# Kernel tuning notes

Measured on AMD Instinct MI355X. Metric: run time of the kernel, lower is better.

Reference implementation:

```python
import jax, jax.numpy as jnp
import numpy as np

N = 50000      # nodes
E = 800000     # edges per view (before self loops)
F_IN = 256     # node feature dim
H = 4          # attention heads
C = 128        # hidden dim (per-head out_channels; concat=False -> mean over heads)
V = 3          # views
NEG_SLOPE = 0.2


def gat_view(x, edge_index, W, a_src, a_dst, b):
    """PyG-style GATConv(heads=H, concat=False) + ELU. Adds self loops."""
    n = x.shape[0]
    loops = jnp.arange(n, dtype=edge_index.dtype)
    src = jnp.concatenate([edge_index[0], loops])  # [E+N]
    dst = jnp.concatenate([edge_index[1], loops])
    h = (x @ W).reshape(n, H, C)                    # [N,H,C]
    s_src = jnp.sum(h * a_src, axis=-1)             # [N,H]
    s_dst = jnp.sum(h * a_dst, axis=-1)             # [N,H]
    e = jax.nn.leaky_relu(s_src[src] + s_dst[dst], NEG_SLOPE)  # [E+N,H]
    # segment softmax over incoming edges of each destination node
    m = jax.ops.segment_max(e, dst, num_segments=n)
    m = jnp.where(jnp.isfinite(m), m, 0.0)
    ex = jnp.exp(e - m[dst])
    denom = jax.ops.segment_sum(ex, dst, num_segments=n)
    alpha = ex / jnp.maximum(denom[dst], 1e-16)     # [E+N,H]
    out = jax.ops.segment_sum(h[src] * alpha[:, :, None], dst, num_segments=n)  # [N,H,C]
    return jax.nn.elu(out.mean(axis=1) + b)         # [N,C]


def setup_inputs() -> dict:
    key = jax.random.key(0)
    ks = jax.random.split(key, 12)
    d = {
        "x": jax.random.normal(ks[0], (N, F_IN), dtype=jnp.float32),
        "edge_index0": jax.random.randint(ks[1], (2, E), 0, N, dtype=jnp.int32),
        "edge_index1": jax.random.randint(ks[2], (2, E), 0, N, dtype=jnp.int32),
        "edge_index2": jax.random.randint(ks[3], (2, E), 0, N, dtype=jnp.int32),
        "W": jax.random.normal(ks[4], (V, F_IN, H * C), dtype=jnp.float32) * 0.05,
        "a_src": jax.random.normal(ks[5], (V, H, C), dtype=jnp.float32) * 0.05,
        "a_dst": jax.random.normal(ks[6], (V, H, C), dtype=jnp.float32) * 0.05,
        "b": jnp.zeros((V, C), dtype=jnp.float32),
        "fus_w": jax.random.normal(ks[7], (C, 1), dtype=jnp.float32) * 0.05,
        "fus_b": jnp.zeros((1,), dtype=jnp.float32),
        "cls_w1": jax.random.normal(ks[8], (C, C // 2), dtype=jnp.float32) * 0.05,
        "cls_b1": jnp.zeros((C // 2,), dtype=jnp.float32),
        "cls_w2": jax.random.normal(ks[9], (C // 2, 2), dtype=jnp.float32) * 0.05,
        "cls_b2": jnp.zeros((2,), dtype=jnp.float32),
    }
    return d


def reference(x, edge_index0, edge_index1, edge_index2, W, a_src, a_dst, b,
              fus_w, fus_b, cls_w1, cls_b1, cls_w2, cls_b2):
    eis = [edge_index0, edge_index1, edge_index2]
    views = [gat_view(x, eis[v], W[v], a_src[v], a_dst[v], b[v]) for v in range(V)]
    stacked = jnp.stack(views, axis=1)                     # [N,V,C]
    scores = jnp.squeeze(stacked @ fus_w, -1) + fus_b      # [N,V]
    weights = jax.nn.softmax(scores, axis=1)               # view attention
    fused = jnp.sum(stacked * weights[..., None], axis=1)  # [N,C]
    hcls = jax.nn.relu(fused @ cls_w1 + cls_b1)            # dropout = identity (eval)
    logits = hcls @ cls_w2 + cls_b2                        # [N,2]
    return logits, weights
```

## Files before the change

### kernel.cpp

```cpp
#include <hip/hip_runtime.h>
#include <math.h>

#define NN 50000
#define EE 800000
#define FIN 256
#define HH 4
#define CC 128
#define HC 512
#define VV 3

#define NB 196
#define SPB 256
#define CAP 4608
#define EPB 2048

typedef __attribute__((ext_vector_type(8))) short short8;
typedef __attribute__((ext_vector_type(4))) float f32x4;
typedef __attribute__((ext_vector_type(2))) float f32x2;

__device__ __forceinline__ float lrelu(float x){ return x > 0.f ? x : 0.2f*x; }

__device__ __forceinline__ unsigned short f2bf(float f){
  unsigned u = __float_as_uint(f);
  u += 0x7fffu + ((u >> 16) & 1);
  return (unsigned short)(u >> 16);
}
__device__ __forceinline__ float bf2f(short b){
  return __uint_as_float(((unsigned)b & 0xffffu) << 16);
}

__device__ __forceinline__ float wave_sum64(float v){
#pragma unroll
  for (int off = 32; off; off >>= 1) v += __shfl_xor(v, off);
  return v;
}

__global__ __launch_bounds__(256) void cast_x(const float* __restrict__ x,
                                              unsigned short* __restrict__ xb){
  int t = blockIdx.x * 256 + threadIdx.x;
  float4 v = *(const float4*)&x[(size_t)t * 4];
  ushort4 o;
  o.x = f2bf(v.x); o.y = f2bf(v.y); o.z = f2bf(v.z); o.w = f2bf(v.w);
  *(ushort4*)&xb[(size_t)t * 4] = o;
}

__global__ __launch_bounds__(256) void prep_w_all(const float* __restrict__ W,
                                                  unsigned short* __restrict__ wp){
  int t = blockIdx.x * 256 + threadIdx.x;
  int v = t >> 17;
  int tl = t & 131071;
  int k = tl >> 9, n = tl & 511;
  wp[(size_t)v * (FIN * HC) + (size_t)(k >> 5) * (HC * 32) + n * 32 + (k & 31)] = f2bf(W[t]);
}

__global__ __launch_bounds__(256) void gemm_mfma_scores(
    const unsigned short* __restrict__ xb, const unsigned short* __restrict__ wp_all,
    unsigned char* __restrict__ hb_all,
    const float* __restrict__ a_src, const float* __restrict__ a_dst,
    float* __restrict__ ssrc_all, float* __restrict__ sdst_all){
  __shared__ float sred[2][128][2];
  int tid = threadIdx.x;
  int wave = tid >> 6, lane = tid & 63;
  int l16 = lane & 15, q = lane >> 4;
  int wr = wave >> 1, wc = wave & 1;
  int head = blockIdx.y, v = blockIdx.z;
  int rowBase = blockIdx.x * 128, colBase = head * 128;

  const unsigned short* wp = wp_all + (size_t)v * FIN * HC;
  unsigned char* hb = hb_all + (size_t)v * NN * HC;
  const float* a_src_v = a_src + v * HH * CC;
  const float* a_dst_v = a_dst + v * HH * CC;
  float* ssrc = ssrc_all + (size_t)v * NN * HH;
  float* sdst = sdst_all + (size_t)v * NN * HH;

  const unsigned short* ap[4];
  const unsigned short* bp[4];
#pragma unroll
  for (int i = 0; i < 4; i++){
    int row = min(rowBase + wr * 64 + i * 16 + l16, NN - 1);
    ap[i] = xb + (size_t)row * FIN + q * 8;
  }
#pragma unroll
  for (int j = 0; j < 4; j++){
    int col = colBase + wc * 64 + j * 16 + l16;
    bp[j] = wp + (size_t)col * 32 + q * 8;
  }
  f32x4 acc[4][4] = {};
#pragma unroll
  for (int kt = 0; kt < 8; kt++){
    short8 af[4], bf[4];
#pragma unroll
    for (int i = 0; i < 4; i++){
      af[i] = *(const short8*)(ap[i] + kt * 32);
      bf[i] = *(const short8*)(bp[i] + (size_t)kt * (HC * 32));
    }
#pragma unroll
    for (int i = 0; i < 4; i++)
#pragma unroll
      for (int j = 0; j < 4; j++)
        acc[i][j] = __builtin_amdgcn_mfma_f32_16x16x32_bf16(af[i], bf[j], acc[i][j], 0, 0, 0);
  }
#pragma unroll
  for (int i = 0; i < 4; i++){
#pragma unroll
    for (int r = 0; r < 4; r++){
      int row = rowBase + wr * 64 + i * 16 + q * 4 + r;
      if (row < NN){
        int p01 = __builtin_amdgcn_cvt_pk_fp8_f32(acc[i][0][r], acc[i][1][r], 0, false);
        int p23 = __builtin_amdgcn_cvt_pk_fp8_f32(acc[i][2][r], acc[i][3][r], 0, false);
        size_t rb = (size_t)row * HC + colBase + wc * 64 + l16;
        hb[rb +  0] = (unsigned char)(p01 & 0xff);
        hb[rb + 16] = (unsigned char)((p01 >> 8) & 0xff);
        hb[rb + 32] = (unsigned char)(p23 & 0xff);
        hb[rb + 48] = (unsigned char)((p23 >> 8) & 0xff);
      }
    }
  }
  float asv[4], adv[4];
#pragma unroll
  for (int j = 0; j < 4; j++){
    int c = wc * 64 + j * 16 + l16;
    asv[j] = a_src_v[head * CC + c];
    adv[j] = a_dst_v[head * CC + c];
  }
  float ps[4][4], pd[4][4];
#pragma unroll
  for (int i = 0; i < 4; i++)
#pragma unroll
    for (int r = 0; r < 4; r++){
      float s = 0.f, d = 0.f;
#pragma unroll
      for (int j = 0; j < 4; j++){
        s = fmaf(acc[i][j][r], asv[j], s);
        d = fmaf(acc[i][j][r], adv[j], d);
      }
      ps[i][r] = s; pd[i][r] = d;
    }
#pragma unroll
  for (int off = 1; off < 16; off <<= 1)
#pragma unroll
    for (int i = 0; i < 4; i++)
#pragma unroll
      for (int r = 0; r < 4; r++){
        ps[i][r] += __shfl_xor(ps[i][r], off);
        pd[i][r] += __shfl_xor(pd[i][r], off);
      }
  if (l16 == 0){
#pragma unroll
    for (int i = 0; i < 4; i++)
#pragma unroll
      for (int r = 0; r < 4; r++){
        int rl = wr * 64 + i * 16 + q * 4 + r;
        sred[wc][rl][0] = ps[i][r];
        sred[wc][rl][1] = pd[i][r];
      }
  }
  __syncthreads();
  if (tid < 128){
    int row = rowBase + tid;
    if (row < NN){
      ssrc[row * HH + head] = sred[0][tid][0] + sred[1][tid][0];
      sdst[row * HH + head] = sred[0][tid][1] + sred[1][tid][1];
    }
  }
}

__global__ __launch_bounds__(256) void bucket_scatter(const int* __restrict__ e0,
    const int* __restrict__ e1, const int* __restrict__ e2,
    int* __restrict__ gcur, unsigned* __restrict__ pairs){
  int v = blockIdx.y;
  const int* ei = (v == 0) ? e0 : ((v == 1) ? e1 : e2);
  __shared__ int cnt[NB];
  __shared__ int base[NB];
  int tid = threadIdx.x;
  for (int i = tid; i < NB; i += 256) cnt[i] = 0;
  __syncthreads();
  int estart = blockIdx.x * EPB;
  int eend = min(estart + EPB, EE);
  for (int e = estart + tid; e < eend; e += 256)
    atomicAdd(&cnt[ei[EE + e] >> 8], 1);
  __syncthreads();
  for (int i = tid; i < NB; i += 256){
    int c = cnt[i];
    base[i] = (c > 0) ? atomicAdd(&gcur[v * NB + i], c) : 0;
    cnt[i] = 0;
  }
  __syncthreads();
  for (int e = estart + tid; e < eend; e += 256){
    int s = ei[e], d = ei[EE + e];
    int b = d >> 8;
    int off = base[b] + atomicAdd(&cnt[b], 1);
    if (off < CAP)
      pairs[(size_t)(v * NB + b) * CAP + off] = ((unsigned)(d & 255) << 16) | (unsigned)s;
  }
}

__global__ __launch_bounds__(256) void bucket_scan(const int* __restrict__ gcur,
                                                   int* __restrict__ bbase){
  int v = blockIdx.x;
  __shared__ int wsum[4];
  int tid = threadIdx.x, lane = tid & 63, wv = tid >> 6;
  int val = 0;
  if (tid < NB) val = min(gcur[v * NB + tid], CAP) + min(SPB, NN - tid * SPB);
  int x = val;
#pragma unroll
  for (int off = 1; off < 64; off <<= 1){
    int t = __shfl_up(x, off);
    if (lane >= off) x += t;
  }
  if (lane == 63) wsum[wv] = x;
  __syncthreads();
  int pre = 0;
#pragma unroll
  for (int w = 0; w < 4; w++) if (w < wv) pre += wsum[w];
  if (tid < NB) bbase[v * NB + tid] = pre + x - val;
}

__global__ __launch_bounds__(256) void bucket_csr(const int* __restrict__ gcur,
    const int* __restrict__ bbase, const unsigned* __restrict__ pairs,
    int* __restrict__ rowptr_all, int* __restrict__ colx_all){
  int v = blockIdx.y, b = blockIdx.x;
  int* rowptr = rowptr_all + v * (NN + 1);
  int* colx = colx_all + (size_t)v * (EE + NN);
  __shared__ int hist[SPB];
  __shared__ int wsum[4];
  __shared__ int lcol[CAP + SPB];
  int tid = threadIdx.x, lane = tid & 63, wv = tid >> 6;
  int node0 = b << 8;
  int nvalid = min(SPB, NN - node0);
  int cnt = min(gcur[v * NB + b], CAP);
  int base = bbase[v * NB + b];
  const unsigned* pp = pairs + (size_t)(v * NB + b) * CAP;
  hist[tid] = (tid < nvalid) ? 1 : 0;
  __syncthreads();
  for (int i = tid; i < cnt; i += 256)
    atomicAdd(&hist[pp[i] >> 16], 1);
  __syncthreads();
  int val = hist[tid];
  int x = val;
#pragma unroll
  for (int off = 1; off < 64; off <<= 1){
    int t = __shfl_up(x, off);
    if (lane >= off) x += t;
  }
  if (lane == 63) wsum[wv] = x;
  __syncthreads();
  int pre = 0;
#pragma unroll
  for (int w = 0; w < 4; w++) if (w < wv) pre += wsum[w];
  int excl = pre + x - val;
  __syncthreads();
  hist[tid] = excl + ((tid < nvalid) ? 1 : 0);
  if (tid < nvalid){
    rowptr[node0 + tid] = base + excl;
    lcol[excl] = node0 + tid;
  }
  __syncthreads();
  for (int i = tid; i < cnt; i += 256){
    unsigned p = pp[i];
    int pos = atomicAdd(&hist[p >> 16], 1);
    lcol[pos] = (int)(p & 0xffffu);
  }
  __syncthreads();
  int total = cnt + nvalid;
  for (int i = tid; i < total; i += 256) colx[base + i] = lcol[i];
  if (b == NB - 1 && tid == 0) rowptr[NN] = base + total;
}

__global__ __launch_bounds__(256) void aggregate(const unsigned char* __restrict__ hb_all,
    const float* __restrict__ ssrc_all, const float* __restrict__ sdst_all,
    const int* __restrict__ rowptr_all, const int* __restrict__ colx_all,
    const float* __restrict__ bb, unsigned short* __restrict__ vout_all){
  int v = blockIdx.y;
  const unsigned char* hb = hb_all + (size_t)v * NN * HC;
  const float* ssrc = ssrc_all + (size_t)v * NN * HH;
  const float* sdst = sdst_all + (size_t)v * NN * HH;
  const int* rowptr = rowptr_all + v * (NN + 1);
  const int* colx = colx_all + (size_t)v * (EE + NN);

  int wave = threadIdx.x >> 6, lane = threadIdx.x & 63;
  int node = blockIdx.x * 4 + wave;
  int start = rowptr[node];
  int deg = rowptr[node + 1] - start;
  int myh = lane >> 4;
  float sdh = sdst[node * HH + myh];
  float acc[8] = {0.f, 0.f, 0.f, 0.f, 0.f, 0.f, 0.f, 0.f};
  float dsum = 0.f;

#define AGG_FMA(CH, CE) { \
    f32x2 p0 = __builtin_amdgcn_cvt_pk_f32_fp8(CH.x, false); \
    f32x2 p1 = __builtin_amdgcn_cvt_pk_f32_fp8(CH.x, true); \
    f32x2 p2 = __builtin_amdgcn_cvt_pk_f32_fp8(CH.y, false); \
    f32x2 p3 = __builtin_amdgcn_cvt_pk_f32_fp8(CH.y, true); \
    acc[0] = fmaf(CE, p0[0], acc[0]); \
    acc[1] = fmaf(CE, p0[1], acc[1]); \
    acc[2] = fmaf(CE, p1[0], acc[2]); \
    acc[3] = fmaf(CE, p1[1], acc[3]); \
    acc[4] = fmaf(CE, p2[0], acc[4]); \
    acc[5] = fmaf(CE, p2[1], acc[5]); \
    acc[6] = fmaf(CE, p3[0], acc[6]); \
    acc[7] = fmaf(CE, p3[1], acc[7]); }

  if (deg <= 64){
    int cpre = (lane < deg) ? colx[start + lane] : 0;
    uint2 h0, h1, h2, h3, h4, h5, h6, h7;
    float s0, s1, s2, s3, s4, s5, s6, s7;
#define AGG_PRO(HP, SP, P) { \
    int sp = __shfl(cpre, min(P, deg - 1)); \
    HP = *(const uint2*)&hb[(size_t)(unsigned)(sp * HC) + lane * 8]; \
    SP = ssrc[sp * HH + myh]; }
    AGG_PRO(h0, s0, 0) AGG_PRO(h1, s1, 1) AGG_PRO(h2, s2, 2) AGG_PRO(h3, s3, 3)
    AGG_PRO(h4, s4, 4) AGG_PRO(h5, s5, 5) AGG_PRO(h6, s6, 6) AGG_PRO(h7, s7, 7)
#undef AGG_PRO
#define AGG_STEP(HP, SP, P) { \
    float ce = __expf(lrelu(SP + sdh)); \
    dsum += ce; \
    uint2 ch = HP; \
    int ni = i + 8 + P; \
    if (ni < deg){ \
      int ns = __shfl(cpre, ni); \
      HP = *(const uint2*)&hb[(size_t)(unsigned)(ns * HC) + lane * 8]; \
      SP = ssrc[ns * HH + myh]; \
    } \
    AGG_FMA(ch, ce) }
    int i = 0;
    for (; i + 8 <= deg; i += 8){
      AGG_STEP(h0, s0, 0) AGG_STEP(h1, s1, 1) AGG_STEP(h2, s2, 2) AGG_STEP(h3, s3, 3)
      AGG_STEP(h4, s4, 4) AGG_STEP(h5, s5, 5) AGG_STEP(h6, s6, 6) AGG_STEP(h7, s7, 7)
    }
#undef AGG_STEP
    int rem = deg - i;
#define AGG_TAIL(HP, SP, P) if (rem > P){ \
    float ce = __expf(lrelu(SP + sdh)); \
    dsum += ce; \
    AGG_FMA(HP, ce) }
    AGG_TAIL(h0, s0, 0) AGG_TAIL(h1, s1, 1) AGG_TAIL(h2, s2, 2) AGG_TAIL(h3, s3, 3)
    AGG_TAIL(h4, s4, 4) AGG_TAIL(h5, s5, 5) AGG_TAIL(h6, s6, 6)
#undef AGG_TAIL
  } else {
    for (int i = 0; i < deg; i++){
      int src = colx[start + i];
      float sv = ssrc[src * HH + myh];
      float ce = __expf(lrelu(sv + sdh));
      dsum += ce;
      uint2 ch = *(const uint2*)&hb[(size_t)(unsigned)(src * HC) + lane * 8];
      AGG_FMA(ch, ce)
    }
  }
#undef AGG_FMA
  float rinv = 0.25f / fmaxf(dsum, 1e-16f);
#pragma unroll
  for (int j = 0; j < 8; j++) acc[j] *= rinv;
#pragma unroll
  for (int off = 16; off < 64; off <<= 1){
#pragma unroll
    for (int j = 0; j < 8; j++) acc[j] += __shfl_xor(acc[j], off);
  }
  if (lane < 16){
    const float* bv = bb + v * CC;
    unsigned short* voutv = vout_all + (size_t)v * NN * CC;
    int c0 = lane * 8;
    short8 o;
#pragma unroll
    for (int j = 0; j < 8; j++){
      float vv = acc[j] + bv[c0 + j];
      float e = vv > 0.f ? vv : (__expf(vv) - 1.f);
      o[j] = (short)f2bf(e);
    }
    *(short8*)&voutv[(size_t)node * CC + c0] = o;
  }
}

__global__ __launch_bounds__(256) void fuse_classify(const unsigned short* __restrict__ vb,
    const float* __restrict__ fw, const float* __restrict__ fb,
    const float* __restrict__ w1, const float* __restrict__ b1,
    const float* __restrict__ w2, const float* __restrict__ b2,
    float* __restrict__ out){
  __shared__ float sw1[CC * 64];
  __shared__ float sfused[4][CC];
  int tid = threadIdx.x;
  for (int i = tid * 4; i < CC * 64; i += 1024)
    *(float4*)&sw1[i] = *(const float4*)&w1[i];
  __syncthreads();
  int wave = tid >> 6, lane = tid & 63;
  float fwa = fw[lane * 2], fwb = fw[lane * 2 + 1];
  float w2a = w2[lane * 2], w2b = w2[lane * 2 + 1];
  float b1l = b1[lane];
  for (int g = 0; g < 8; g++){
    int node = blockIdx.x * 32 + g * 4 + wave;
    if (node < NN){
      unsigned r0 = *(const unsigned*)&vb[(size_t)(0 * NN + node) * CC + lane * 2];
      unsigned r1 = *(const unsigned*)&vb[(size_t)(1 * NN + node) * CC + lane * 2];
      unsigned r2 = *(const unsigned*)&vb[(size_t)(2 * NN + node) * CC + lane * 2];
      float v0x = bf2f((short)(r0 & 0xffffu)), v0y = bf2f((short)(r0 >> 16));
      float v1x = bf2f((short)(r1 & 0xffffu)), v1y = bf2f((short)(r1 >> 16));
      float v2x = bf2f((short)(r2 & 0xffffu)), v2y = bf2f((short)(r2 >> 16));
      float s0 = wave_sum64(v0x * fwa + v0y * fwb) + fb[0];
      float s1 = wave_sum64(v1x * fwa + v1y * fwb) + fb[0];
      float s2 = wave_sum64(v2x * fwa + v2y * fwb) + fb[0];
      float mx = fmaxf(s0, fmaxf(s1, s2));
      float e0 = __expf(s0 - mx), e1 = __expf(s1 - mx), e2 = __expf(s2 - mx);
      float rs = 1.f / (e0 + e1 + e2);
      float w0 = e0 * rs, w1v = e1 * rs, w2v = e2 * rs;
      float f0 = w0 * v0x + w1v * v1x + w2v * v2x;
      float f1 = w0 * v0y + w1v * v1y + w2v * v2y;
      sfused[wave][lane * 2]     = f0;
      sfused[wave][lane * 2 + 1] = f1;
      if (lane < 3){
        float wv = (lane == 0) ? w0 : ((lane == 1) ? w1v : w2v);
        out[2 * NN + node * 3 + lane] = wv;
      }
      __builtin_amdgcn_s_waitcnt(0);
      float hc = b1l;
#pragma unroll 8
      for (int c = 0; c < CC; c++)
        hc = fmaf(sfused[wave][c], sw1[c * 64 + lane], hc);
      hc = fmaxf(hc, 0.f);
      float l0 = wave_sum64(hc * w2a);
      float l1 = wave_sum64(hc * w2b);
      if (lane == 0){
        out[node * 2]     = l0 + b2[0];
        out[node * 2 + 1] = l1 + b2[1];
      }
    }
  }
}

extern "C" void kernel_launch(void* const* d_in, const int* in_sizes, int n_in,
                              void* d_out, int out_size, void* d_ws, size_t ws_size,
                              hipStream_t stream){
  const float* x      = (const float*)d_in[0];
  const int*   e0     = (const int*)d_in[1];
  const int*   e1     = (const int*)d_in[2];
  const int*   e2     = (const int*)d_in[3];
  const float* W      = (const float*)d_in[4];
  const float* a_src  = (const float*)d_in[5];
  const float* a_dst  = (const float*)d_in[6];
  const float* bb     = (const float*)d_in[7];
  const float* fus_w  = (const float*)d_in[8];
  const float* fus_b  = (const float*)d_in[9];
  const float* cls_w1 = (const float*)d_in[10];
  const float* cls_b1 = (const float*)d_in[11];
  const float* cls_w2 = (const float*)d_in[12];
  const float* cls_b2 = (const float*)d_in[13];
  float* out = (float*)d_out;

  unsigned short* xb = (unsigned short*)d_ws;
  unsigned char* hb  = (unsigned char*)(xb + (size_t)NN * FIN);
  unsigned short* wp = (unsigned short*)(hb + (size_t)VV * NN * HC);
  float* ssrc = (float*)(wp + (size_t)VV * FIN * HC);
  float* sdst = ssrc + (size_t)VV * NN * HH;
  int* gcur   = (int*)(sdst + (size_t)VV * NN * HH);
  int* bbase  = gcur + VV * NB;
  int* rowptr = bbase + VV * NB;
  int* colx   = rowptr + VV * (NN + 1);
  unsigned* pairs = (unsigned*)(colx + (size_t)VV * (EE + NN));
  unsigned short* voutb = (unsigned short*)pairs;

  hipMemsetAsync(gcur, 0, (size_t)VV * NB * sizeof(int), stream);
  cast_x<<<12500, 256, 0, stream>>>(x, xb);
  prep_w_all<<<1536, 256, 0, stream>>>(W, wp);
  dim3 p1grid((EE + EPB - 1) / EPB, 3);
  bucket_scatter<<<p1grid, 256, 0, stream>>>(e0, e1, e2, gcur, pairs);
  bucket_scan<<<3, 256, 0, stream>>>(gcur, bbase);
  dim3 p2grid(NB, 3);
  bucket_csr<<<p2grid, 256, 0, stream>>>(gcur, bbase, pairs, rowptr, colx);

  dim3 ggrid(391, 4, 3);
  gemm_mfma_scores<<<ggrid, 256, 0, stream>>>(xb, wp, hb, a_src, a_dst, ssrc, sdst);
  dim3 agrid(12500, 3);
  aggregate<<<agrid, 256, 0, stream>>>(hb, ssrc, sdst, rowptr, colx, bb, voutb);
  fuse_classify<<<1563, 256, 0, stream>>>(voutb, fus_w, fus_b, cls_w1, cls_b1,
                                          cls_w2, cls_b2, out);
}
```

Baseline: 582.4 us.

## Loop over heads in GEMM block to reuse A fragments in registers

The scores GEMM now loads a block's x rows once into registers (all 8 k-tiles) and loops over the 4 heads inside the block, so the grid shrinks from 391x4x3 to 391x3. B fragments are double-buffered across k-tiles so the next tile's load overlaps the current MFMAs, and launch bounds request 2 blocks per SIMD. This removes the 4x re-reading of A per row tile. In exchange it uses more registers, gives fewer blocks for latency hiding, and adds extra barriers per head.

```diff
diff --git a/kernel.cpp b/kernel.cpp
--- a/kernel.cpp
+++ b/kernel.cpp
@@ -53,7 +53,7 @@
   wp[(size_t)v * (FIN * HC) + (size_t)(k >> 5) * (HC * 32) + n * 32 + (k & 31)] = f2bf(W[t]);
 }
 
-__global__ __launch_bounds__(256) void gemm_mfma_scores(
+__global__ __launch_bounds__(256, 2) void gemm_mfma_scores(
     const unsigned short* __restrict__ xb, const unsigned short* __restrict__ wp_all,
     unsigned char* __restrict__ hb_all,
     const float* __restrict__ a_src, const float* __restrict__ a_dst,
@@ -63,104 +63,111 @@
   int wave = tid >> 6, lane = tid & 63;
   int l16 = lane & 15, q = lane >> 4;
   int wr = wave >> 1, wc = wave & 1;
-  int head = blockIdx.y, v = blockIdx.z;
-  int rowBase = blockIdx.x * 128, colBase = head * 128;
+  int v = blockIdx.y;
+  int rowBase = blockIdx.x * 128;
 
   const unsigned short* wp = wp_all + (size_t)v * FIN * HC;
   unsigned char* hb = hb_all + (size_t)v * NN * HC;
-  const float* a_src_v = a_src + v * HH * CC;
-  const float* a_dst_v = a_dst + v * HH * CC;
   float* ssrc = ssrc_all + (size_t)v * NN * HH;
   float* sdst = sdst_all + (size_t)v * NN * HH;
 
-  const unsigned short* ap[4];
-  const unsigned short* bp[4];
+  short8 af[8][4];
 #pragma unroll
   for (int i = 0; i < 4; i++){
     int row = min(rowBase + wr * 64 + i * 16 + l16, NN - 1);
-    ap[i] = xb + (size_t)row * FIN + q * 8;
-  }
-#pragma unroll
-  for (int j = 0; j < 4; j++){
-    int col = colBase + wc * 64 + j * 16 + l16;
-    bp[j] = wp + (size_t)col * 32 + q * 8;
-  }
-  f32x4 acc[4][4] = {};
-#pragma unroll
-  for (int kt = 0; kt < 8; kt++){
-    short8 af[4], bf[4];
+    const unsigned short* aprow = xb + (size_t)row * FIN + q * 8;
+#pragma unroll
+    for (int kt = 0; kt < 8; kt++)
+      af[kt][i] = *(const short8*)(aprow + kt * 32);
+  }
+
+  for (int head = 0; head < HH; head++){
+    int colBase = head * 128;
+    const unsigned short* bp[4];
+#pragma unroll
+    for (int j = 0; j < 4; j++)
+      bp[j] = wp + (size_t)(colBase + wc * 64 + j * 16 + l16) * 32 + q * 8;
+    f32x4 acc[4][4] = {};
+    short8 bf[2][4];
+#pragma unroll
+    for (int j = 0; j < 4; j++) bf[0][j] = *(const short8*)(bp[j]);
+#pragma unroll
+    for (int kt = 0; kt < 8; kt++){
+      int cur = kt & 1, nxt = cur ^ 1;
+      if (kt < 7){
+#pragma unroll
+        for (int j = 0; j < 4; j++)
+          bf[nxt][j] = *(const short8*)(bp[j] + (size_t)(kt + 1) * (HC * 32));
+      }
+#pragma unroll
+      for (int i = 0; i < 4; i++)
+#pragma unroll
+        for (int j = 0; j < 4; j++)
+          acc[i][j] = __builtin_amdgcn_mfma_f32_16x16x32_bf16(af[kt][i], bf[cur][j], acc[i][j], 0, 0, 0);
+    }
 #pragma unroll
     for (int i = 0; i < 4; i++){
-      af[i] = *(const short8*)(ap[i] + kt * 32);
-      bf[i] = *(const short8*)(bp[i] + (size_t)kt * (HC * 32));
-    }
+#pragma unroll
+      for (int r = 0; r < 4; r++){
+        int row = rowBase + wr * 64 + i * 16 + q * 4 + r;
+        if (row < NN){
+          int p01 = __builtin_amdgcn_cvt_pk_fp8_f32(acc[i][0][r], acc[i][1][r], 0, false);
+          int p23 = __builtin_amdgcn_cvt_pk_fp8_f32(acc[i][2][r], acc[i][3][r], 0, false);
+          size_t rb = (size_t)row * HC + colBase + wc * 64 + l16;
+          hb[rb +  0] = (unsigned char)(p01 & 0xff);
+          hb[rb + 16] = (unsigned char)((p01 >> 8) & 0xff);
+          hb[rb + 32] = (unsigned char)(p23 & 0xff);
+          hb[rb + 48] = (unsigned char)((p23 >> 8) & 0xff);
+        }
+      }
+    }
+    float asv[4], adv[4];
+#pragma unroll
+    for (int j = 0; j < 4; j++){
+      int c = wc * 64 + j * 16 + l16;
+      asv[j] = a_src[(v * HH + head) * CC + c];
+      adv[j] = a_dst[(v * HH + head) * CC + c];
+    }
+    float ps[4][4], pd[4][4];
 #pragma unroll
     for (int i = 0; i < 4; i++)
 #pragma unroll
-      for (int j = 0; j < 4; j++)
-        acc[i][j] = __builtin_amdgcn_mfma_f32_16x16x32_bf16(af[i], bf[j], acc[i][j], 0, 0, 0);
-  }
-#pragma unroll
-  for (int i = 0; i < 4; i++){
-#pragma unroll
-    for (int r = 0; r < 4; r++){
-      int row = rowBase + wr * 64 + i * 16 + q * 4 + r;
+      for (int r = 0; r < 4; r++){
+        float s = 0.f, d = 0.f;
+#pragma unroll
+        for (int j = 0; j < 4; j++){
+          s = fmaf(acc[i][j][r], asv[j], s);
+          d = fmaf(acc[i][j][r], adv[j], d);
+        }
+        ps[i][r] = s; pd[i][r] = d;
+      }
+#pragma unroll
+    for (int off = 1; off < 16; off <<= 1)
+#pragma unroll
+      for (int i = 0; i < 4; i++)
+#pragma unroll
+        for (int r = 0; r < 4; r++){
+          ps[i][r] += __shfl_xor(ps[i][r], off);
+          pd[i][r] += __shfl_xor(pd[i][r], off);
+        }
+    __syncthreads();
+    if (l16 == 0){
+#pragma unroll
+      for (int i = 0; i < 4; i++)
+#pragma unroll
+        for (int r = 0; r < 4; r++){
+          int rl = wr * 64 + i * 16 + q * 4 + r;
+          sred[wc][rl][0] = ps[i][r];
+          sred[wc][rl][1] = pd[i][r];
+        }
+    }
+    __syncthreads();
+    if (tid < 128){
+      int row = rowBase + tid;
       if (row < NN){
-        int p01 = __builtin_amdgcn_cvt_pk_fp8_f32(acc[i][0][r], acc[i][1][r], 0, false);
-        int p23 = __builtin_amdgcn_cvt_pk_fp8_f32(acc[i][2][r], acc[i][3][r], 0, false);
-        size_t rb = (size_t)row * HC + colBase + wc * 64 + l16;
-        hb[rb +  0] = (unsigned char)(p01 & 0xff);
-        hb[rb + 16] = (unsigned char)((p01 >> 8) & 0xff);
-        hb[rb + 32] = (unsigned char)(p23 & 0xff);
-        hb[rb + 48] = (unsigned char)((p23 >> 8) & 0xff);
-      }
-    }
-  }
-  float asv[4], adv[4];
-#pragma unroll
-  for (int j = 0; j < 4; j++){
-    int c = wc * 64 + j * 16 + l16;
-    asv[j] = a_src_v[head * CC + c];
-    adv[j] = a_dst_v[head * CC + c];
-  }
-  float ps[4][4], pd[4][4];
-#pragma unroll
-  for (int i = 0; i < 4; i++)
-#pragma unroll
-    for (int r = 0; r < 4; r++){
-      float s = 0.f, d = 0.f;
-#pragma unroll
-      for (int j = 0; j < 4; j++){
-        s = fmaf(acc[i][j][r], asv[j], s);
-        d = fmaf(acc[i][j][r], adv[j], d);
-      }
-      ps[i][r] = s; pd[i][r] = d;
-    }
-#pragma unroll
-  for (int off = 1; off < 16; off <<= 1)
-#pragma unroll
-    for (int i = 0; i < 4; i++)
-#pragma unroll
-      for (int r = 0; r < 4; r++){
-        ps[i][r] += __shfl_xor(ps[i][r], off);
-        pd[i][r] += __shfl_xor(pd[i][r], off);
-      }
-  if (l16 == 0){
-#pragma unroll
-    for (int i = 0; i < 4; i++)
-#pragma unroll
-      for (int r = 0; r < 4; r++){
-        int rl = wr * 64 + i * 16 + q * 4 + r;
-        sred[wc][rl][0] = ps[i][r];
-        sred[wc][rl][1] = pd[i][r];
-      }
-  }
-  __syncthreads();
-  if (tid < 128){
-    int row = rowBase + tid;
-    if (row < NN){
-      ssrc[row * HH + head] = sred[0][tid][0] + sred[1][tid][0];
-      sdst[row * HH + head] = sred[0][tid][1] + sred[1][tid][1];
+        ssrc[row * HH + head] = sred[0][tid][0] + sred[1][tid][0];
+        sdst[row * HH + head] = sred[0][tid][1] + sred[1][tid][1];
+      }
     }
   }
 }
@@ -466,7 +473,7 @@
   dim3 p2grid(NB, 3);
   bucket_csr<<<p2grid, 256, 0, stream>>>(gcur, bbase, pairs, rowptr, colx);
 
-  dim3 ggrid(391, 4, 3);
+  dim3 ggrid(391, 3);
   gemm_mfma_scores<<<ggrid, 256, 0, stream>>>(xb, wp, hb, a_src, a_dst, ssrc, sdst);
   dim3 agrid(12500, 3);
   aggregate<<<agrid, 256, 0, stream>>>(hb, ssrc, sdst, rowptr, colx, bb, voutb);
```

Result: faster. 546.3 us (-6.2%).
